# Kernel optimization log

Measured on AMD Instinct MI355X. Metric: run time of the kernel, lower is better.

The kernel has to match this reference:

```python
import jax, jax.numpy as jnp
import numpy as np

N_NODES = 100000
N_EDGES = 1600000
D = 128          # gnn_input_size == gnn_hidden_size
N_LAYERS = 7
N_GRAPHS = 64
N_CLASSES = 10
SNN_IN, SNN_H = 512, 1024
SNN_BETA = 0.85


def setup_inputs() -> dict:
    key = jax.random.key(0)
    ks = jax.random.split(key, 16)
    s = 0.05  # keep activations tame through 7 relu layers
    return {
        "snn_x": jax.random.normal(ks[0], (N_GRAPHS, SNN_IN), jnp.float32),
        "x": jax.random.normal(ks[1], (N_NODES, D), jnp.float32),
        "edge_index": jax.random.randint(ks[2], (2, N_EDGES), 0, N_NODES, jnp.int64),
        "batch": jnp.sort(jax.random.randint(ks[3], (N_NODES,), 0, N_GRAPHS, jnp.int64)),
        "snn_w1": jax.random.normal(ks[4], (SNN_IN, SNN_H), jnp.float32) * s,
        "snn_b1": jax.random.normal(ks[5], (SNN_H,), jnp.float32) * s,
        "snn_w2": jax.random.normal(ks[6], (SNN_H, N_CLASSES), jnp.float32) * s,
        "snn_b2": jax.random.normal(ks[7], (N_CLASSES,), jnp.float32) * s,
        "conv_wrel": jax.random.normal(ks[8], (N_LAYERS, D, D), jnp.float32) * s,
        "conv_wroot": jax.random.normal(ks[9], (N_LAYERS, D, D), jnp.float32) * s,
        "conv_brel": jax.random.normal(ks[10], (N_LAYERS, D), jnp.float32) * s,
        "lin_w": jax.random.normal(ks[11], (D, N_CLASSES), jnp.float32) * s,
        "lin_b": jax.random.normal(ks[12], (N_CLASSES,), jnp.float32) * s,
        "fuse_w": jax.random.normal(ks[13], (2 * N_CLASSES, N_CLASSES), jnp.float32) * s,
        "fuse_b": jax.random.normal(ks[14], (N_CLASSES,), jnp.float32) * s,
    }


def reference(snn_x, x, edge_index, batch,
              snn_w1, snn_b1, snn_w2, snn_b2,
              conv_wrel, conv_wroot, conv_brel,
              lin_w, lin_b, fuse_w, fuse_b):
    n = x.shape[0]
    src, dst = edge_index[0], edge_index[1]
    h = x
    for i in range(conv_wrel.shape[0]):
        agg = jax.ops.segment_sum(h[src], dst, num_segments=n)  # gather + scatter-add
        h = jax.nn.relu(agg @ conv_wrel[i] + conv_brel[i] + h @ conv_wroot[i])
    # global_mean_pool over batch segments
    sums = jax.ops.segment_sum(h, batch, num_segments=N_GRAPHS)
    cnts = jax.ops.segment_sum(jnp.ones((n,), h.dtype), batch, num_segments=N_GRAPHS)
    pooled = sums / jnp.maximum(cnts, 1.0)[:, None]
    gnn_logits = pooled @ lin_w + lin_b
    # SNN branch
    snn_h = jax.nn.relu(snn_x @ snn_w1 + snn_b1)
    snn_logits = SNN_BETA * (snn_h @ snn_w2 + snn_b2)
    # fusion
    fused = jnp.concatenate([snn_logits, gnn_logits], axis=-1)
    return fused @ fuse_w + fuse_b
```

## Files before the change

kernel.cpp:

```cpp
#include <hip/hip_runtime.h>
#include <hip/hip_bf16.h>

#define N_NODES 100000
#define N_EDGES 1600000
#define DIM     128
#define N_LAYERS 7
#define N_GRAPHS 64
#define SNN_IN  512
#define SNN_HID 1024
#define NCLS    10
#define M_PAD   100096
#define MBLK    782
#define NBK     782
#define SORT_CHUNK 4096
#define SORT_NCH   391
#define XPAIRS  (N_NODES * 64)
#define HPAIRS  (M_PAD * 64)
#define WELEMS  (N_LAYERS * DIM * 256)
#define AGG_BLOCKS 2048
#define AGG_WAVES  (AGG_BLOCKS * 4)
#define NQUAD   (N_NODES / 4)
#define POOL_NB 782
#define SS_PAD  2000384

typedef __attribute__((ext_vector_type(8))) short short8;
typedef __attribute__((ext_vector_type(4))) float f32x4;

__device__ __forceinline__ unsigned int f2bf(float f) {
    unsigned int u = __float_as_uint(f);
    return (u + 0x7fffu + ((u >> 16) & 1u)) >> 16;
}
__device__ __forceinline__ float bf2f(unsigned short b) {
    return __uint_as_float(((unsigned int)b) << 16);
}
__device__ __forceinline__ void acc_pair(unsigned int u, float& lo, float& hi) {
    lo += __uint_as_float(u << 16);
    hi += __uint_as_float(u & 0xffff0000u);
}

__global__ void k_convert(const float* __restrict__ x, const float* __restrict__ wrel,
                          const float* __restrict__ wroot, unsigned int* __restrict__ h,
                          unsigned short* __restrict__ Wt,
                          float* __restrict__ pooled, int* __restrict__ counts) {
    int i = blockIdx.x * blockDim.x + threadIdx.x;
    if (i < N_GRAPHS * 128) pooled[i] = 0.f;
    if (i >= N_GRAPHS * 128 && i < N_GRAPHS * 129) counts[i - N_GRAPHS * 128] = 0;
    if (i < XPAIRS) {
        float2 v = ((const float2*)x)[i];
        h[i] = f2bf(v.x) | (f2bf(v.y) << 16);
    } else if (i < HPAIRS) {
        h[i] = 0u;
    } else {
        int idx = i - HPAIRS;
        if (idx < WELEMS) {
            int l = idx >> 15, rem = idx & 32767, n = rem >> 8, k = rem & 255;
            float v = (k < 128) ? wrel[l * 16384 + k * 128 + n]
                                : wroot[l * 16384 + (k - 128) * 128 + n];
            Wt[idx] = (unsigned short)f2bf(v);
        }
    }
}

__global__ __launch_bounds__(256) void k_histA(const int* __restrict__ dst,
                                               int* __restrict__ chunk_hist) {
    __shared__ int hist[NBK];
    int b = blockIdx.x, t = threadIdx.x;
    int e0 = b * SORT_CHUNK;
    int e1 = e0 + SORT_CHUNK; if (e1 > N_EDGES) e1 = N_EDGES;
    for (int i = t; i < NBK; i += 256) hist[i] = 0;
    __syncthreads();
    for (int e = e0 + t; e < e1; e += 256) atomicAdd(&hist[dst[e] >> 7], 1);
    __syncthreads();
    for (int i = t; i < NBK; i += 256) chunk_hist[b * NBK + i] = hist[i];
}

__global__ __launch_bounds__(64) void k_colscan(int* __restrict__ chunk_hist,
                                                int* __restrict__ btot) {
    int b = blockIdx.x;
    int lane = threadIdx.x;
    const int C = (SORT_NCH + 63) / 64;
    int vals[C]; int sum = 0;
    #pragma unroll
    for (int j = 0; j < C; j++) {
        int c = lane * C + j;
        vals[j] = (c < SORT_NCH) ? chunk_hist[c * NBK + b] : 0;
        sum += vals[j];
    }
    int s = sum;
    #pragma unroll
    for (int o = 1; o < 64; o <<= 1) { int t = __shfl_up(s, o); if (lane >= o) s += t; }
    if (lane == 63) btot[b] = s;
    int run = s - sum;
    #pragma unroll
    for (int j = 0; j < C; j++) {
        int c = lane * C + j;
        if (c < SORT_NCH) chunk_hist[c * NBK + b] = run;
        run += vals[j];
    }
}

__global__ __launch_bounds__(256) void k_bscan(const int* __restrict__ btot,
                                               int* __restrict__ bucket_base) {
    __shared__ int wsum[4];
    int tid = threadIdx.x, lane = tid & 63, wid = tid >> 6;
    int i0 = tid * 4;
    int v[4]; int sum = 0;
    #pragma unroll
    for (int j = 0; j < 4; j++) { int i = i0 + j; v[j] = (i < NBK) ? btot[i] : 0; sum += v[j]; }
    int s = sum;
    #pragma unroll
    for (int o = 1; o < 64; o <<= 1) { int t = __shfl_up(s, o); if (lane >= o) s += t; }
    if (lane == 63) wsum[wid] = s;
    __syncthreads();
    if (tid == 0) {
        int acc = 0;
        #pragma unroll
        for (int w = 0; w < 4; w++) { acc += wsum[w]; wsum[w] = acc; }
    }
    __syncthreads();
    int prefix = s - sum + (wid ? wsum[wid - 1] : 0);
    #pragma unroll
    for (int j = 0; j < 4; j++) { int i = i0 + j; if (i < NBK) bucket_base[i] = prefix; prefix += v[j]; }
}

__global__ __launch_bounds__(256) void k_scatterA(const int* __restrict__ src,
                                                  const int* __restrict__ dst,
                                                  const int* __restrict__ chunk_hist,
                                                  const int* __restrict__ bucket_base,
                                                  unsigned int* __restrict__ pairs) {
    __shared__ int lcur[NBK];
    int b = blockIdx.x, t = threadIdx.x;
    int e0 = b * SORT_CHUNK;
    int e1 = e0 + SORT_CHUNK; if (e1 > N_EDGES) e1 = N_EDGES;
    for (int i = t; i < NBK; i += 256) lcur[i] = chunk_hist[b * NBK + i] + bucket_base[i];
    __syncthreads();
    for (int e = e0 + t; e < e1; e += 256) {
        int d = dst[e];
        int bk = d >> 7;
        int pos = atomicAdd(&lcur[bk], 1);
        pairs[pos] = (unsigned int)src[e] | ((unsigned int)(d & 127) << 17);
    }
}

__global__ __launch_bounds__(256) void k_bucketB(const unsigned int* __restrict__ pairs,
                                                 const int* __restrict__ bucket_base,
                                                 const int* __restrict__ btot,
                                                 int* __restrict__ row_off,
                                                 int* __restrict__ ndeg,
                                                 int* __restrict__ sorted_src) {
    __shared__ int lcnt[128];
    __shared__ int loff[128];
    int b = blockIdx.x, t = threadIdx.x;
    int node0 = b << 7;
    int nn = N_NODES - node0; if (nn > 128) nn = 128;
    int base = bucket_base[b];
    int end  = base + btot[b];
    int pbase = ((base + 3) & ~3) + 512 * b;
    if (t < 128) lcnt[t] = 0;
    __syncthreads();
    for (int i = base + t; i < end; i += 256) atomicAdd(&lcnt[pairs[i] >> 17], 1);
    __syncthreads();
    if (t < 64) {
        int v0 = (lcnt[2 * t] + 3) & ~3, v1 = (lcnt[2 * t + 1] + 3) & ~3;
        int s = v0 + v1, ps = s;
        #pragma unroll
        for (int o = 1; o < 64; o <<= 1) { int u = __shfl_up(ps, o); if (t >= o) ps += u; }
        int excl = ps - s;
        loff[2 * t] = excl; loff[2 * t + 1] = excl + v0;
    }
    __syncthreads();
    if (t < nn) {
        int d = lcnt[t];
        row_off[node0 + t] = pbase + loff[t];
        ndeg[node0 + t] = d;
        int pad = (d + 3) & ~3;
        for (int k = d; k < pad; k++) sorted_src[pbase + loff[t] + k] = N_NODES;
    }
    __syncthreads();
    if (t < 128) lcnt[t] = 0;
    __syncthreads();
    for (int i = base + t; i < end; i += 256) {
        unsigned int p = pairs[i];
        int l = p >> 17;
        int pos = atomicAdd(&lcnt[l], 1);
        sorted_src[pbase + loff[l] + pos] = (int)(p & 0x1FFFFu);
    }
}

#define GATH(d0, d1, d2, d3, s) \
    d0 = *(const uint4*)(hbl + (size_t)(((unsigned)(s).x) << 8)); \
    d1 = *(const uint4*)(hbl + (size_t)(((unsigned)(s).y) << 8)); \
    d2 = *(const uint4*)(hbl + (size_t)(((unsigned)(s).z) << 8)); \
    d3 = *(const uint4*)(hbl + (size_t)(((unsigned)(s).w) << 8));
#define ACC4(r0, r1, r2, r3) \
    acc_pair((r0).x, a[0], a[1]); acc_pair((r0).y, a[2], a[3]); \
    acc_pair((r0).z, a[4], a[5]); acc_pair((r0).w, a[6], a[7]); \
    acc_pair((r1).x, a[0], a[1]); acc_pair((r1).y, a[2], a[3]); \
    acc_pair((r1).z, a[4], a[5]); acc_pair((r1).w, a[6], a[7]); \
    acc_pair((r2).x, a[0], a[1]); acc_pair((r2).y, a[2], a[3]); \
    acc_pair((r2).z, a[4], a[5]); acc_pair((r2).w, a[6], a[7]); \
    acc_pair((r3).x, a[0], a[1]); acc_pair((r3).y, a[2], a[3]); \
    acc_pair((r3).z, a[4], a[5]); acc_pair((r3).w, a[6], a[7]);

__global__ __launch_bounds__(256) void k_agg(const char* __restrict__ hb,
                                             const int* __restrict__ row_off,
                                             const int* __restrict__ ndeg,
                                             const int4* __restrict__ sorted4,
                                             uint4* __restrict__ agg4) {
    int gw = blockIdx.x * 4 + (threadIdx.x >> 6);
    int lane = threadIdx.x & 63;
    int sub = lane >> 4, li = lane & 15;
    const char* hbl = hb + li * 16;
    for (int quad = gw; quad < NQUAD; quad += AGG_WAVES) {
        int node = quad * 4 + sub;
        int beg = row_off[node] >> 2;
        int nit = (ndeg[node] + 3) >> 2;
        float a[8] = {0.f, 0.f, 0.f, 0.f, 0.f, 0.f, 0.f, 0.f};
        if (nit > 0) {
            int4 sa = sorted4[beg];
            int4 sb = sorted4[beg + 1];
            uint4 A0, A1, A2, A3, B0, B1, B2, B3;
            GATH(A0, A1, A2, A3, sa);
            int it = 0;
            for (; it + 2 < nit; it += 2) {
                GATH(B0, B1, B2, B3, sb);
                sa = sorted4[beg + it + 2];
                ACC4(A0, A1, A2, A3);
                GATH(A0, A1, A2, A3, sa);
                sb = sorted4[beg + it + 3];
                ACC4(B0, B1, B2, B3);
            }
            if (it + 1 < nit) {
                GATH(B0, B1, B2, B3, sb);
                ACC4(A0, A1, A2, A3);
                ACC4(B0, B1, B2, B3);
            } else {
                ACC4(A0, A1, A2, A3);
            }
        }
        uint4 o;
        o.x = f2bf(a[0]) | (f2bf(a[1]) << 16);
        o.y = f2bf(a[2]) | (f2bf(a[3]) << 16);
        o.z = f2bf(a[4]) | (f2bf(a[5]) << 16);
        o.w = f2bf(a[6]) | (f2bf(a[7]) << 16);
        agg4[(size_t)node * 16 + li] = o;
    }
}

__global__ __launch_bounds__(256) void k_gemm(const unsigned short* __restrict__ Ag,
                                              const unsigned short* __restrict__ H,
                                              const unsigned short* __restrict__ Wt,
                                              const float* __restrict__ bias,
                                              unsigned short* __restrict__ Hout) {
    __shared__ unsigned short Es[64 * 144];
    int tid = threadIdx.x;
    int lane = tid & 63, wid = tid >> 6;
    int wr = (wid >> 1) * 64, wc = (wid & 1) * 64;
    int row0 = blockIdx.x * 128;
    f32x4 acc[4][4] = {};

    int ksub = (lane >> 4) * 8;
    const unsigned short* Aga = Ag + (size_t)(row0 + wr + (lane & 15)) * 128 + ksub;
    const unsigned short* Ha  = H  + (size_t)(row0 + wr + (lane & 15)) * 128 + ksub;
    const unsigned short* Bb  = Wt + (size_t)(wc + (lane & 15)) * 256 + ksub;

    auto load_frags = [&](short8* a, short8* b, int s) {
        const unsigned short* ab = (s < 4 ? Aga : Ha) + (s & 3) * 32;
        #pragma unroll
        for (int mi = 0; mi < 4; mi++) a[mi] = *(const short8*)(ab + mi * 16 * 128);
        const unsigned short* bp = Bb + s * 32;
        #pragma unroll
        for (int ni = 0; ni < 4; ni++) b[ni] = *(const short8*)(bp + ni * 16 * 256);
    };
    auto do_mfma = [&](short8* a, short8* b) {
        #pragma unroll
        for (int mi = 0; mi < 4; mi++)
            #pragma unroll
            for (int ni = 0; ni < 4; ni++)
                acc[mi][ni] = __builtin_amdgcn_mfma_f32_16x16x32_bf16(a[mi], b[ni], acc[mi][ni], 0, 0, 0);
    };

    short8 a0[4], b0[4], a1[4], b1[4];
    load_frags(a0, b0, 0);
    #pragma unroll
    for (int s = 0; s < 8; s += 2) {
        load_frags(a1, b1, s + 1);
        do_mfma(a0, b0);
        if (s + 2 < 8) load_frags(a0, b0, s + 2);
        do_mfma(a1, b1);
    }

    int cb = wc + (lane & 15);
    int rs = (lane >> 4) * 4;
    #pragma unroll
    for (int p = 0; p < 2; ++p) {
        __syncthreads();
        if (wr == 64 * p) {
            #pragma unroll
            for (int ni = 0; ni < 4; ni++) {
                int col = cb + ni * 16;
                float bn = bias[col];
                #pragma unroll
                for (int mi = 0; mi < 4; mi++) {
                    int rloc = mi * 16 + rs;
                    #pragma unroll
                    for (int rr = 0; rr < 4; rr++) {
                        float v = acc[mi][ni][rr] + bn;
                        v = v > 0.f ? v : 0.f;
                        if (row0 + 64 * p + rloc + rr >= N_NODES) v = 0.f;
                        Es[(rloc + rr) * 144 + col] = (unsigned short)f2bf(v);
                    }
                }
            }
        }
        __syncthreads();
        int rloc = tid >> 2;
        int c4 = (tid & 3) * 4;
        uint4* gd = (uint4*)(Hout + (size_t)(row0 + 64 * p + rloc) * 128);
        const uint4* es = (const uint4*)(Es + (size_t)rloc * 144);
        #pragma unroll
        for (int j = 0; j < 4; j++) gd[c4 + j] = es[c4 + j];
    }
}

__global__ __launch_bounds__(256) void k_pool_snn(const unsigned short* __restrict__ h,
                                                  const int* __restrict__ batch,
                                                  float* __restrict__ pooled,
                                                  int* __restrict__ counts,
                                                  const float* __restrict__ x,
                                                  const float* __restrict__ w1,
                                                  const float* __restrict__ b1,
                                                  float* __restrict__ snn_out) {
    if (blockIdx.x < POOL_NB) {
        __shared__ int bsh[128];
        int start = blockIdx.x * 128;
        int t = threadIdx.x & 127;
        int half = threadIdx.x >> 7;
        if (half == 0) {
            int end = start + 128; if (end > N_NODES) end = N_NODES;
            int nn = end - start;
            if (t < nn) bsh[t] = batch[start + t];
        }
        __syncthreads();
        if (half == 1) {
            int end = start + 128; if (end > N_NODES) end = N_NODES;
            int nn = end - start;
            float acc = 0.f; int cur = -1, cnt = 0;
            for (int i = 0; i < nn; i++) {
                int g = bsh[i];
                if (g != cur) {
                    if (cur >= 0) { atomicAdd(&pooled[cur * 128 + t], acc); if (t == 0) atomicAdd(&counts[cur], cnt); }
                    cur = g; acc = 0.f; cnt = 0;
                }
                acc += bf2f(h[(size_t)(start + i) * 128 + t]);
                cnt++;
            }
            if (cur >= 0) { atomicAdd(&pooled[cur * 128 + t], acc); if (t == 0) atomicAdd(&counts[cur], cnt); }
        }
    } else {
        int m = blockIdx.x - POOL_NB;
        __shared__ float xs[SNN_IN];
        int tid = threadIdx.x;
        for (int i = tid; i < SNN_IN; i += 256) xs[i] = x[m * SNN_IN + i];
        __syncthreads();
        float a0 = 0.f, a1 = 0.f, a2 = 0.f, a3 = 0.f;
        for (int k = 0; k < SNN_IN; k++) {
            float xv = xs[k];
            const float* wr = w1 + (size_t)k * SNN_HID + tid;
            a0 += xv * wr[0]; a1 += xv * wr[256]; a2 += xv * wr[512]; a3 += xv * wr[768];
        }
        float v;
        v = a0 + b1[tid];       snn_out[m * SNN_HID + tid]       = v > 0.f ? v : 0.f;
        v = a1 + b1[tid + 256]; snn_out[m * SNN_HID + tid + 256] = v > 0.f ? v : 0.f;
        v = a2 + b1[tid + 512]; snn_out[m * SNN_HID + tid + 512] = v > 0.f ? v : 0.f;
        v = a3 + b1[tid + 768]; snn_out[m * SNN_HID + tid + 768] = v > 0.f ? v : 0.f;
    }
}

__global__ __launch_bounds__(64) void k_head(const float* __restrict__ pooled, const int* __restrict__ counts,
                                             const float* __restrict__ lin_w, const float* __restrict__ lin_b,
                                             const float* __restrict__ snn_h, const float* __restrict__ w2,
                                             const float* __restrict__ b2, const float* __restrict__ fuse_w,
                                             const float* __restrict__ fuse_b, float* __restrict__ out) {
    int m = blockIdx.x, lane = threadIdx.x;
    __shared__ float sm[20];
    float cnt = (float)(counts[m] > 0 ? counts[m] : 1);
    float p0 = pooled[m * 128 + lane] / cnt;
    float p1 = pooled[m * 128 + 64 + lane] / cnt;
    for (int c = 0; c < NCLS; c++) {
        float v = p0 * lin_w[lane * 10 + c] + p1 * lin_w[(lane + 64) * 10 + c];
        #pragma unroll
        for (int o = 32; o > 0; o >>= 1) v += __shfl_down(v, o);
        if (lane == 0) sm[10 + c] = v + lin_b[c];
    }
    for (int c = 0; c < NCLS; c++) {
        float v = 0.f;
        #pragma unroll
        for (int j = 0; j < 16; j++) {
            int k = lane + j * 64;
            v += snn_h[m * SNN_HID + k] * w2[k * 10 + c];
        }
        #pragma unroll
        for (int o = 32; o > 0; o >>= 1) v += __shfl_down(v, o);
        if (lane == 0) sm[c] = 0.85f * (v + b2[c]);
    }
    __syncthreads();
    if (lane < NCLS) {
        float o = fuse_b[lane];
        #pragma unroll
        for (int j = 0; j < 20; j++) o += sm[j] * fuse_w[j * 10 + lane];
        out[m * 10 + lane] = o;
    }
}

extern "C" void kernel_launch(void* const* d_in, const int* in_sizes, int n_in,
                              void* d_out, int out_size, void* d_ws, size_t ws_size,
                              hipStream_t stream) {
    const float* snn_x  = (const float*)d_in[0];
    const float* x      = (const float*)d_in[1];
    const int*   ei     = (const int*)d_in[2];
    const int*   batch  = (const int*)d_in[3];
    const float* w1     = (const float*)d_in[4];
    const float* b1     = (const float*)d_in[5];
    const float* w2     = (const float*)d_in[6];
    const float* b2     = (const float*)d_in[7];
    const float* wrel   = (const float*)d_in[8];
    const float* wroot  = (const float*)d_in[9];
    const float* brel   = (const float*)d_in[10];
    const float* lin_w  = (const float*)d_in[11];
    const float* lin_b  = (const float*)d_in[12];
    const float* fuse_w = (const float*)d_in[13];
    const float* fuse_b = (const float*)d_in[14];
    const int* srcv = ei;
    const int* dstv = ei + N_EDGES;

    char* ws = (char*)d_ws;
    size_t off = 0;
    auto alloc = [&](size_t b) { char* p = ws + off; off = (off + b + 255) & ~(size_t)255; return p; };
    unsigned short* h0   = (unsigned short*)alloc((size_t)M_PAD * 128 * 2);
    unsigned short* h1   = (unsigned short*)alloc((size_t)M_PAD * 128 * 2);
    unsigned short* agg  = (unsigned short*)alloc((size_t)M_PAD * 128 * 2);
    unsigned short* Wt   = (unsigned short*)alloc((size_t)N_LAYERS * 128 * 256 * 2);
    int* sorted_src = (int*)alloc((size_t)SS_PAD * 4 + 16);
    unsigned int* pairs = (unsigned int*)alloc((size_t)N_EDGES * 4);
    int* chunk_hist = (int*)alloc((size_t)SORT_NCH * NBK * 4);
    int* row_off    = (int*)alloc((size_t)(N_NODES + 1) * 4);
    int* ndeg       = (int*)alloc((size_t)N_NODES * 4);
    int* btot       = (int*)alloc((size_t)NBK * 4);
    int* bucket_base= (int*)alloc((size_t)NBK * 4);
    float* pooled   = (float*)alloc((size_t)N_GRAPHS * 128 * 4);
    int* counts     = (int*)alloc((size_t)N_GRAPHS * 4);
    float* snn_h    = (float*)alloc((size_t)N_GRAPHS * SNN_HID * 4);

    k_histA<<<SORT_NCH, 256, 0, stream>>>(dstv, chunk_hist);
    k_colscan<<<NBK, 64, 0, stream>>>(chunk_hist, btot);
    k_bscan<<<1, 256, 0, stream>>>(btot, bucket_base);
    k_scatterA<<<SORT_NCH, 256, 0, stream>>>(srcv, dstv, chunk_hist, bucket_base, pairs);
    k_bucketB<<<NBK, 256, 0, stream>>>(pairs, bucket_base, btot, row_off, ndeg, sorted_src);
    k_convert<<<(HPAIRS + WELEMS + 255) / 256, 256, 0, stream>>>(x, wrel, wroot, (unsigned int*)h0,
                                                                 Wt, pooled, counts);

    unsigned short* hc = h0;
    unsigned short* hn = h1;
    for (int l = 0; l < N_LAYERS; l++) {
        k_agg<<<AGG_BLOCKS, 256, 0, stream>>>((const char*)hc, row_off, ndeg,
                                              (const int4*)sorted_src, (uint4*)agg);
        k_gemm<<<MBLK, 256, 0, stream>>>(agg, hc, Wt + (size_t)l * 128 * 256, brel + l * 128, hn);
        unsigned short* t = hc; hc = hn; hn = t;
    }
    k_pool_snn<<<POOL_NB + N_GRAPHS, 256, 0, stream>>>(hc, batch, pooled, counts,
                                                       snn_x, w1, b1, snn_h);
    k_head<<<N_GRAPHS, 64, 0, stream>>>(pooled, counts, lin_w, lin_b, snn_h, w2, b2, fuse_w, fuse_b,
                                        (float*)d_out);
}
```

Measured before the change: 932.5 us.

## Fuse neighbor aggregation and GraphConv GEMM into one per-layer kernel

Merges the gather/scatter aggregation kernel and the MFMA GEMM kernel into a single kernel that handles a 64-row tile. Aggregated rows stay in swizzled LDS instead of a global agg buffer, and the root H tile is loaded into LDS asynchronously with global_load_lds. This removes the global write and reread of the agg array and halves the per-layer launches. In exchange, weight fragments are read straight from global memory on every block, there is no persistent grid-stride loop, and the LDS use of 32KB per block may limit occupancy during the latency-bound gather.

```diff
diff --git a/kernel.cpp b/kernel.cpp
--- a/kernel.cpp
+++ b/kernel.cpp
@@ -10,18 +10,18 @@
 #define SNN_HID 1024
 #define NCLS    10
 #define M_PAD   100096
-#define MBLK    782
 #define NBK     782
 #define SORT_CHUNK 4096
 #define SORT_NCH   391
 #define XPAIRS  (N_NODES * 64)
 #define HPAIRS  (M_PAD * 64)
 #define WELEMS  (N_LAYERS * DIM * 256)
-#define AGG_BLOCKS 2048
-#define AGG_WAVES  (AGG_BLOCKS * 4)
-#define NQUAD   (N_NODES / 4)
 #define POOL_NB 782
 #define SS_PAD  2000384
+#define FBLK    1564
+
+#define AS1 __attribute__((address_space(1)))
+#define AS3 __attribute__((address_space(3)))
 
 typedef __attribute__((ext_vector_type(8))) short short8;
 typedef __attribute__((ext_vector_type(4))) float f32x4;
@@ -202,19 +202,37 @@
     acc_pair((r3).x, a[0], a[1]); acc_pair((r3).y, a[2], a[3]); \
     acc_pair((r3).z, a[4], a[5]); acc_pair((r3).w, a[6], a[7]);
 
-__global__ __launch_bounds__(256) void k_agg(const char* __restrict__ hb,
-                                             const int* __restrict__ row_off,
-                                             const int* __restrict__ ndeg,
-                                             const int4* __restrict__ sorted4,
-                                             uint4* __restrict__ agg4) {
-    int gw = blockIdx.x * 4 + (threadIdx.x >> 6);
-    int lane = threadIdx.x & 63;
+__global__ __launch_bounds__(256) void k_layer(const char* __restrict__ hb,
+                                               const int* __restrict__ row_off,
+                                               const int* __restrict__ ndeg,
+                                               const int4* __restrict__ sorted4,
+                                               const unsigned short* __restrict__ WtL,
+                                               const float* __restrict__ bias,
+                                               unsigned short* __restrict__ Hout) {
+    __shared__ char smem[32768];
+    int tid = threadIdx.x, lane = tid & 63, wid = tid >> 6;
     int sub = lane >> 4, li = lane & 15;
+    int row0 = blockIdx.x * 64;
+    char* aggS = smem;
+    char* Hs = smem + 16384;
+
+    #pragma unroll
+    for (int j = 0; j < 4; j++) {
+        int lrow = 16 * wid + 4 * j + sub;
+        int schunk = li ^ (lrow & 7);
+        const char* g = hb + (size_t)(row0 + lrow) * 256 + schunk * 16;
+        char* ldst = Hs + (16 * wid + 4 * j) * 256;
+        __builtin_amdgcn_global_load_lds((const AS1 unsigned int*)g,
+                                         (AS3 unsigned int*)ldst, 16, 0, 0);
+    }
+    __builtin_amdgcn_sched_barrier(0);
+
     const char* hbl = hb + li * 16;
-    for (int quad = gw; quad < NQUAD; quad += AGG_WAVES) {
-        int node = quad * 4 + sub;
-        int beg = row_off[node] >> 2;
-        int nit = (ndeg[node] + 3) >> 2;
+    for (int j = 0; j < 4; j++) {
+        int lrow = 16 * wid + 4 * j + sub;
+        int node = row0 + lrow;
+        int beg = 0, nit = 0;
+        if (node < N_NODES) { beg = row_off[node] >> 2; nit = (ndeg[node] + 3) >> 2; }
         float a[8] = {0.f, 0.f, 0.f, 0.f, 0.f, 0.f, 0.f, 0.f};
         if (nit > 0) {
             int4 sa = sorted4[beg];
@@ -243,83 +261,49 @@
         o.y = f2bf(a[2]) | (f2bf(a[3]) << 16);
         o.z = f2bf(a[4]) | (f2bf(a[5]) << 16);
         o.w = f2bf(a[6]) | (f2bf(a[7]) << 16);
-        agg4[(size_t)node * 16 + li] = o;
-    }
-}
-
-__global__ __launch_bounds__(256) void k_gemm(const unsigned short* __restrict__ Ag,
-                                              const unsigned short* __restrict__ H,
-                                              const unsigned short* __restrict__ Wt,
-                                              const float* __restrict__ bias,
-                                              unsigned short* __restrict__ Hout) {
-    __shared__ unsigned short Es[64 * 144];
-    int tid = threadIdx.x;
-    int lane = tid & 63, wid = tid >> 6;
-    int wr = (wid >> 1) * 64, wc = (wid & 1) * 64;
-    int row0 = blockIdx.x * 128;
-    f32x4 acc[4][4] = {};
-
-    int ksub = (lane >> 4) * 8;
-    const unsigned short* Aga = Ag + (size_t)(row0 + wr + (lane & 15)) * 128 + ksub;
-    const unsigned short* Ha  = H  + (size_t)(row0 + wr + (lane & 15)) * 128 + ksub;
-    const unsigned short* Bb  = Wt + (size_t)(wc + (lane & 15)) * 256 + ksub;
-
-    auto load_frags = [&](short8* a, short8* b, int s) {
-        const unsigned short* ab = (s < 4 ? Aga : Ha) + (s & 3) * 32;
-        #pragma unroll
-        for (int mi = 0; mi < 4; mi++) a[mi] = *(const short8*)(ab + mi * 16 * 128);
-        const unsigned short* bp = Bb + s * 32;
-        #pragma unroll
-        for (int ni = 0; ni < 4; ni++) b[ni] = *(const short8*)(bp + ni * 16 * 256);
-    };
-    auto do_mfma = [&](short8* a, short8* b) {
-        #pragma unroll
-        for (int mi = 0; mi < 4; mi++)
-            #pragma unroll
-            for (int ni = 0; ni < 4; ni++)
-                acc[mi][ni] = __builtin_amdgcn_mfma_f32_16x16x32_bf16(a[mi], b[ni], acc[mi][ni], 0, 0, 0);
-    };
-
-    short8 a0[4], b0[4], a1[4], b1[4];
-    load_frags(a0, b0, 0);
-    #pragma unroll
-    for (int s = 0; s < 8; s += 2) {
-        load_frags(a1, b1, s + 1);
-        do_mfma(a0, b0);
-        if (s + 2 < 8) load_frags(a0, b0, s + 2);
-        do_mfma(a1, b1);
-    }
-
-    int cb = wc + (lane & 15);
-    int rs = (lane >> 4) * 4;
-    #pragma unroll
-    for (int p = 0; p < 2; ++p) {
-        __syncthreads();
-        if (wr == 64 * p) {
-            #pragma unroll
-            for (int ni = 0; ni < 4; ni++) {
-                int col = cb + ni * 16;
-                float bn = bias[col];
-                #pragma unroll
-                for (int mi = 0; mi < 4; mi++) {
-                    int rloc = mi * 16 + rs;
-                    #pragma unroll
-                    for (int rr = 0; rr < 4; rr++) {
-                        float v = acc[mi][ni][rr] + bn;
-                        v = v > 0.f ? v : 0.f;
-                        if (row0 + 64 * p + rloc + rr >= N_NODES) v = 0.f;
-                        Es[(rloc + rr) * 144 + col] = (unsigned short)f2bf(v);
-                    }
-                }
-            }
-        }
-        __syncthreads();
-        int rloc = tid >> 2;
-        int c4 = (tid & 3) * 4;
-        uint4* gd = (uint4*)(Hout + (size_t)(row0 + 64 * p + rloc) * 128);
-        const uint4* es = (const uint4*)(Es + (size_t)rloc * 144);
-        #pragma unroll
-        for (int j = 0; j < 4; j++) gd[c4 + j] = es[c4 + j];
+        int schunk = li ^ (lrow & 7);
+        *(uint4*)(aggS + lrow * 256 + schunk * 16) = o;
+    }
+
+    asm volatile("s_waitcnt vmcnt(0)" ::: "memory");
+    __builtin_amdgcn_sched_barrier(0);
+
+    f32x4 acc[8] = {(f32x4){0,0,0,0}, (f32x4){0,0,0,0}, (f32x4){0,0,0,0}, (f32x4){0,0,0,0},
+                    (f32x4){0,0,0,0}, (f32x4){0,0,0,0}, (f32x4){0,0,0,0}, (f32x4){0,0,0,0}};
+    int r = 16 * wid + li;
+    #pragma unroll
+    for (int sg = 0; sg < 8; sg++) {
+        const char* panel = (sg < 4) ? aggS : Hs;
+        int c = ((sg & 3) * 4 + sub) ^ (r & 7);
+        short8 av = *(const short8*)(panel + r * 256 + c * 16);
+        #pragma unroll
+        for (int ni = 0; ni < 8; ni++) {
+            short8 bv = *(const short8*)(WtL + (size_t)(ni * 16 + li) * 256 + sg * 32 + sub * 8);
+            acc[ni] = __builtin_amdgcn_mfma_f32_16x16x32_bf16(av, bv, acc[ni], 0, 0, 0);
+        }
+    }
+
+    #pragma unroll
+    for (int ni = 0; ni < 8; ni++) {
+        float bn = bias[ni * 16 + li];
+        #pragma unroll
+        for (int rr = 0; rr < 4; rr++) {
+            int lrow = 16 * wid + 4 * sub + rr;
+            float v = acc[ni][rr] + bn;
+            v = v > 0.f ? v : 0.f;
+            if (row0 + lrow >= N_NODES) v = 0.f;
+            int cb = ni * 32 + li * 2;
+            int ch = (cb >> 4) ^ (lrow & 7);
+            *(unsigned short*)(aggS + lrow * 256 + ch * 16 + (cb & 15)) = (unsigned short)f2bf(v);
+        }
+    }
+    #pragma unroll
+    for (int j = 0; j < 4; j++) {
+        int lrow = 16 * wid + (lane >> 2);
+        int cout = (lane & 3) * 4 + j;
+        int c = cout ^ (lrow & 7);
+        uint4 v = *(const uint4*)(aggS + lrow * 256 + c * 16);
+        *(uint4*)((char*)Hout + (size_t)(row0 + lrow) * 256 + cout * 16) = v;
     }
 }
 
@@ -439,7 +423,6 @@
     auto alloc = [&](size_t b) { char* p = ws + off; off = (off + b + 255) & ~(size_t)255; return p; };
     unsigned short* h0   = (unsigned short*)alloc((size_t)M_PAD * 128 * 2);
     unsigned short* h1   = (unsigned short*)alloc((size_t)M_PAD * 128 * 2);
-    unsigned short* agg  = (unsigned short*)alloc((size_t)M_PAD * 128 * 2);
     unsigned short* Wt   = (unsigned short*)alloc((size_t)N_LAYERS * 128 * 256 * 2);
     int* sorted_src = (int*)alloc((size_t)SS_PAD * 4 + 16);
     unsigned int* pairs = (unsigned int*)alloc((size_t)N_EDGES * 4);
@@ -463,9 +446,9 @@
     unsigned short* hc = h0;
     unsigned short* hn = h1;
     for (int l = 0; l < N_LAYERS; l++) {
-        k_agg<<<AGG_BLOCKS, 256, 0, stream>>>((const char*)hc, row_off, ndeg,
-                                              (const int4*)sorted_src, (uint4*)agg);
-        k_gemm<<<MBLK, 256, 0, stream>>>(agg, hc, Wt + (size_t)l * 128 * 256, brel + l * 128, hn);
+        k_layer<<<FBLK, 256, 0, stream>>>((const char*)hc, row_off, ndeg,
+                                          (const int4*)sorted_src,
+                                          Wt + (size_t)l * 128 * 256, brel + l * 128, hn);
         unsigned short* t = hc; hc = hn; hn = t;
     }
     k_pool_snn<<<POOL_NB + N_GRAPHS, 256, 0, stream>>>(hc, batch, pooled, counts,
```

Measured after the change: 962.8 us. +3.3%, slower.
